# Kernel tuning notes

Measured on AMD Instinct MI355X. Metric: run time of the kernel, lower is better.

Reference implementation:

```python
import jax, jax.numpy as jnp
import numpy as np

HEADS1, HID1 = 4, 64   # layer 1: concat -> 256
HEADS2, HID2 = 1, 64   # layer 2: out_channels
NEG_SLOPE = 0.2


def gat_layer(x_src, x_dst, W_src, W_dst, att_src, att_dst, bias, src, dst, n_tgt, heads, hid):
    # bipartite GATConv (PyG math), concat heads
    xs = (x_src @ W_src).reshape(-1, heads, hid)          # [Ns,H,C]
    xd = (x_dst @ W_dst).reshape(-1, heads, hid)          # [Nt,H,C]
    a_s = jnp.sum(xs * att_src, axis=-1)                  # [Ns,H]
    a_d = jnp.sum(xd * att_dst, axis=-1)                  # [Nt,H]
    e = jax.nn.leaky_relu(a_s[src] + a_d[dst], NEG_SLOPE) # [E,H]
    m = jax.ops.segment_max(e, dst, num_segments=n_tgt)
    m = jnp.where(jnp.isfinite(m), m, 0.0)
    ex = jnp.exp(e - m[dst])
    denom = jax.ops.segment_sum(ex, dst, num_segments=n_tgt)
    alpha = ex / (denom[dst] + 1e-16)                     # edge softmax per target
    msg = xs[src] * alpha[:, :, None]                     # [E,H,C]
    out = jax.ops.segment_sum(msg, dst, num_segments=n_tgt)
    return out.reshape(n_tgt, heads * hid) + bias


def setup_inputs() -> dict:
    key = jax.random.key(0)
    ks = jax.random.split(key, 20)
    N0, NT1, NT2 = 100000, 25000, 5000
    E1, E2 = 400000, 100000
    IN, H1 = 256, HEADS1 * HID1  # 256
    OUT = HEADS2 * HID2          # 64
    g = lambda k, sh, fan: jax.random.normal(k, sh, jnp.float32) * (1.0 / np.sqrt(fan))
    return {
        'x': jax.random.normal(ks[0], (N0, IN), jnp.float32),
        'src1': jax.random.randint(ks[1], (E1,), 0, N0),
        'dst1': jax.random.randint(ks[2], (E1,), 0, NT1),
        'src2': jax.random.randint(ks[3], (E2,), 0, NT1),
        'dst2': jax.random.randint(ks[4], (E2,), 0, NT2),
        'n_tgt1': NT1, 'n_tgt2': NT2,
        'W1_src': g(ks[5], (IN, H1), IN), 'W1_dst': g(ks[6], (IN, H1), IN),
        'att1_src': g(ks[7], (HEADS1, HID1), HID1), 'att1_dst': g(ks[8], (HEADS1, HID1), HID1),
        'bias1': jnp.zeros((H1,), jnp.float32),
        'skip1_W': g(ks[9], (IN, H1), IN), 'skip1_b': jnp.zeros((H1,), jnp.float32),
        'W2_src': g(ks[10], (H1, OUT), H1), 'W2_dst': g(ks[11], (H1, OUT), H1),
        'att2_src': g(ks[12], (HEADS2, HID2), HID2), 'att2_dst': g(ks[13], (HEADS2, HID2), HID2),
        'bias2': jnp.zeros((OUT,), jnp.float32),
        'skip2_W': g(ks[14], (H1, OUT), H1), 'skip2_b': jnp.zeros((OUT,), jnp.float32),
    }


def reference(x, src1, dst1, src2, dst2, n_tgt1, n_tgt2,
              W1_src, W1_dst, att1_src, att1_dst, bias1, skip1_W, skip1_b,
              W2_src, W2_dst, att2_src, att2_dst, bias2, skip2_W, skip2_b):
    # layer 1: conv + skip + elu (dropout inactive in eval)
    x_t1 = x[:n_tgt1]
    h = gat_layer(x, x_t1, W1_src, W1_dst, att1_src, att1_dst, bias1,
                  src1, dst1, n_tgt1, HEADS1, HID1)
    h = h + (x_t1 @ skip1_W + skip1_b)
    h = jax.nn.elu(h)
    # layer 2 (final): conv + skip, then log_softmax
    x_t2 = h[:n_tgt2]
    o = gat_layer(h, x_t2, W2_src, W2_dst, att2_src, att2_dst, bias2,
                  src2, dst2, n_tgt2, HEADS2, HID2)
    o = o + (x_t2 @ skip2_W + skip2_b)
    return jax.nn.log_softmax(o, axis=-1)
```

## Files before the change

### kernel.cpp

```cpp
#include <hip/hip_runtime.h>
#include <hip/hip_bf16.h>

using bf16 = __hip_bfloat16;
typedef __attribute__((ext_vector_type(8))) short short8;
typedef __attribute__((ext_vector_type(4))) short short4v;
typedef __attribute__((ext_vector_type(4))) float float4v;

__device__ __forceinline__ short f2bs(float x) {
    bf16 b = __float2bfloat16(x);
    return __builtin_bit_cast(short, b);
}
__device__ __forceinline__ float bs2f(short s) {
    return __uint_as_float(((unsigned)(unsigned short)s) << 16);
}
__device__ __forceinline__ void glds16(const void* g, void* l) {
    __builtin_amdgcn_global_load_lds(
        (const __attribute__((address_space(1))) unsigned int*)g,
        (__attribute__((address_space(3))) unsigned int*)l, 16, 0, 0);
}

__global__ __launch_bounds__(256) void gemm_l1(
        const float* __restrict__ A, const bf16* __restrict__ Bt,
        bf16* __restrict__ xs1, bf16* __restrict__ sk1,
        float* __restrict__ as1, float* __restrict__ ad1,
        const float* __restrict__ att_s, const float* __restrict__ att_d,
        int M, int NT) {
    __shared__ short lds[16 * 512];
    __shared__ float red[128][2];
    const int y = blockIdx.y;
    const int row0 = blockIdx.x * 128;
    if (y >= 2 && row0 >= NT) return;
    const int col0 = y * 128;
    const int tid = threadIdx.x;
    const int wave = tid >> 6, lane = tid & 63;
    const int quad = lane >> 4, l16 = lane & 15;
    const int wr = wave >> 1, wc = wave & 1;

    const float4v fz = {0.f, 0.f, 0.f, 0.f};
    float4v acc[4][4];
#pragma unroll
    for (int i = 0; i < 4; i++)
#pragma unroll
        for (int j = 0; j < 4; j++) acc[i][j] = fz;

    for (int kit = 0; kit < 8; kit++) {
        const int k0 = kit * 32;
        float4v f0[2], f1[2];
#pragma unroll
        for (int i = 0; i < 2; i++) {
            int ar = row0 + (wave * 2 + i) * 16 + l16;
            ar = ar < M ? ar : M - 1;
            const float4v* p = (const float4v*)&A[(size_t)ar * 256 + k0 + quad * 8];
            f0[i] = p[0];
            f1[i] = p[1];
        }
#pragma unroll
        for (int i = 0; i < 2; i++) {
            int bb = wave * 2 + i;
            int brow = col0 + bb * 16 + l16;
            glds16(&Bt[(size_t)brow * 256 + k0 + quad * 8], &lds[(8 + bb) * 512]);
        }
#pragma unroll
        for (int i = 0; i < 2; i++) {
            short8 v;
#pragma unroll
            for (int j = 0; j < 4; j++) { v[j] = f2bs(f0[i][j]); v[4 + j] = f2bs(f1[i][j]); }
            *(short8*)&lds[(wave * 2 + i) * 512 + lane * 8] = v;
        }
        __syncthreads();
        short8 afr[4], bfr[4];
#pragma unroll
        for (int mi = 0; mi < 4; mi++)
            afr[mi] = *(short8*)&lds[(wr * 4 + mi) * 512 + lane * 8];
#pragma unroll
        for (int ni = 0; ni < 4; ni++)
            bfr[ni] = *(short8*)&lds[(8 + wc * 4 + ni) * 512 + lane * 8];
#pragma unroll
        for (int mi = 0; mi < 4; mi++)
#pragma unroll
            for (int ni = 0; ni < 4; ni++)
                acc[mi][ni] = __builtin_amdgcn_mfma_f32_16x16x32_bf16(
                    afr[mi], bfr[ni], acc[mi][ni], 0, 0, 0);
        __syncthreads();
    }

    if (y < 4) {
        const float* attc = y < 2 ? att_s : att_d;
        const int hb = (y < 2 ? y * 2 : (y - 2) * 2) + wc;
        float av[4];
#pragma unroll
        for (int ni = 0; ni < 4; ni++) av[ni] = attc[hb * 64 + ni * 16 + l16];
#pragma unroll
        for (int mi = 0; mi < 4; mi++) {
#pragma unroll
            for (int r = 0; r < 4; r++) {
                float t = acc[mi][0][r] * av[0] + acc[mi][1][r] * av[1] +
                          acc[mi][2][r] * av[2] + acc[mi][3][r] * av[3];
                t += __shfl_xor(t, 1, 64);
                t += __shfl_xor(t, 2, 64);
                t += __shfl_xor(t, 4, 64);
                t += __shfl_xor(t, 8, 64);
                if (l16 == 0) red[wr * 64 + mi * 16 + quad * 4 + r][wc] = t;
            }
        }
        __syncthreads();
        const int aM = y < 2 ? M : NT;
        float* aout = y < 2 ? as1 : ad1;
        const int hbase = y < 2 ? y * 2 : (y - 2) * 2;
        int rl = tid >> 1, gl = tid & 1;
        int grow = row0 + rl;
        if (grow < aM) aout[(size_t)grow * 4 + hbase + gl] = red[rl][gl];
    }

    if (y < 2) {
#pragma unroll
        for (int mi = 0; mi < 4; mi++)
#pragma unroll
            for (int ni = 0; ni < 4; ni++) {
                int col = col0 + wc * 64 + ni * 16 + l16;
#pragma unroll
                for (int r = 0; r < 4; r++) {
                    int row = row0 + wr * 64 + mi * 16 + quad * 4 + r;
                    if (row < M)
                        xs1[(size_t)row * 256 + col] = __float2bfloat16(acc[mi][ni][r]);
                }
            }
    } else if (y >= 4) {
#pragma unroll
        for (int mi = 0; mi < 4; mi++)
#pragma unroll
            for (int ni = 0; ni < 4; ni++) {
                int scol = col0 - 512 + wc * 64 + ni * 16 + l16;
#pragma unroll
                for (int r = 0; r < 4; r++) {
                    int row = row0 + wr * 64 + mi * 16 + quad * 4 + r;
                    if (row < NT)
                        sk1[(size_t)row * 256 + scol] = __float2bfloat16(acc[mi][ni][r]);
                }
            }
    }
}

__global__ __launch_bounds__(256) void gemm_l2(
        const bf16* __restrict__ Ah, const bf16* __restrict__ Bt,
        float* __restrict__ x2, float* __restrict__ a2,
        const float* __restrict__ attc, int NT) {
    __shared__ short lds[12 * 512];
    __shared__ float red[128];
    const int y = blockIdx.y;
    const int row0 = blockIdx.x * 128;
    const int col0 = y * 64;
    const int tid = threadIdx.x;
    const int wave = tid >> 6, lane = tid & 63;
    const int quad = lane >> 4, l16 = lane & 15;

    const float4v fz = {0.f, 0.f, 0.f, 0.f};
    float4v acc[2][4];
#pragma unroll
    for (int i = 0; i < 2; i++)
#pragma unroll
        for (int j = 0; j < 4; j++) acc[i][j] = fz;

    for (int kit = 0; kit < 8; kit++) {
        const int k0 = kit * 32;
#pragma unroll
        for (int i = 0; i < 3; i++) {
            int b = wave * 3 + i;
            if (b < 8) {
                glds16(&Ah[(size_t)(row0 + b * 16 + l16) * 256 + k0 + quad * 8],
                       &lds[b * 512]);
            } else {
                int bb = b - 8;
                glds16(&Bt[(size_t)(col0 + bb * 16 + l16) * 256 + k0 + quad * 8],
                       &lds[b * 512]);
            }
        }
        __syncthreads();
        short8 afr[2], bfr[4];
#pragma unroll
        for (int mi = 0; mi < 2; mi++)
            afr[mi] = *(short8*)&lds[(wave * 2 + mi) * 512 + lane * 8];
#pragma unroll
        for (int ni = 0; ni < 4; ni++)
            bfr[ni] = *(short8*)&lds[(8 + ni) * 512 + lane * 8];
#pragma unroll
        for (int mi = 0; mi < 2; mi++)
#pragma unroll
            for (int ni = 0; ni < 4; ni++)
                acc[mi][ni] = __builtin_amdgcn_mfma_f32_16x16x32_bf16(
                    afr[mi], bfr[ni], acc[mi][ni], 0, 0, 0);
        __syncthreads();
    }

    if (y < 2) {
        float av[4];
#pragma unroll
        for (int ni = 0; ni < 4; ni++) av[ni] = attc[y * 64 + ni * 16 + l16];
#pragma unroll
        for (int mi = 0; mi < 2; mi++) {
#pragma unroll
            for (int r = 0; r < 4; r++) {
                float t = acc[mi][0][r] * av[0] + acc[mi][1][r] * av[1] +
                          acc[mi][2][r] * av[2] + acc[mi][3][r] * av[3];
                t += __shfl_xor(t, 1, 64);
                t += __shfl_xor(t, 2, 64);
                t += __shfl_xor(t, 4, 64);
                t += __shfl_xor(t, 8, 64);
                if (l16 == 0) red[wave * 32 + mi * 16 + quad * 4 + r] = t;
            }
        }
        __syncthreads();
        if (tid < 128) {
            int grow = row0 + tid;
            if (grow < NT) a2[(size_t)grow * 2 + y] = red[tid];
        }
    }
#pragma unroll
    for (int mi = 0; mi < 2; mi++)
#pragma unroll
        for (int ni = 0; ni < 4; ni++) {
            int col = col0 + ni * 16 + l16;
#pragma unroll
            for (int r = 0; r < 4; r++) {
                int row = row0 + wave * 32 + mi * 16 + quad * 4 + r;
                if (row < NT) x2[(size_t)row * 192 + col] = acc[mi][ni][r];
            }
        }
}

__global__ void prep_all(const float* __restrict__ W1s, const float* __restrict__ W1d,
                         const float* __restrict__ W1sk, const float* __restrict__ W2s,
                         const float* __restrict__ W2d, const float* __restrict__ W2sk,
                         const float* __restrict__ a2s, const float* __restrict__ a2d,
                         bf16* __restrict__ Wt1, bf16* __restrict__ Wt2,
                         float* __restrict__ at2c, int* __restrict__ fills, int nfill) {
    int t = blockIdx.x * blockDim.x + threadIdx.x;
    if (t < 196608) {
        int n = t >> 8, k = t & 255;
        const float* W = n < 256 ? W1s : (n < 512 ? W1d : W1sk);
        Wt1[t] = __float2bfloat16(W[k * 256 + (n & 255)]);
    } else if (t < 245760) {
        int i = t - 196608;
        int n = i >> 8, k = i & 255;
        const float* W = n < 64 ? W2s : (n < 128 ? W2d : W2sk);
        Wt2[i] = __float2bfloat16(W[k * 64 + (n & 63)]);
    } else if (t < 245888) {
        int i = t - 245760;
        at2c[i] = i < 64 ? a2s[i] : a2d[i - 64];
    } else if (t < 245888 + nfill) {
        fills[t - 245888] = 0;
    }
}

__global__ void bucket_scatter(const int* __restrict__ s1, const int* __restrict__ d1, int E1,
                               const int* __restrict__ s2, const int* __restrict__ d2, int E2,
                               int* __restrict__ fill1, int* __restrict__ fill2,
                               int* __restrict__ psrc1, int* __restrict__ psrc2) {
    int t = blockIdx.x * blockDim.x + threadIdx.x;
    if (t < E1) {
        int d = d1[t];
        int pos = atomicAdd(&fill1[d], 1);
        if (pos < 64) psrc1[(d << 6) + pos] = s1[t];
    } else if (t < E1 + E2) {
        int tt = t - E1;
        int d = d2[tt];
        int pos = atomicAdd(&fill2[d], 1);
        if (pos < 64) psrc2[(d << 6) + pos] = s2[tt];
    }
}

__global__ __launch_bounds__(256) void agg_h4(
        const int* __restrict__ fill, const int* __restrict__ psrc,
        const bf16* __restrict__ X, const float* __restrict__ as1,
        const float* __restrict__ ad1, const float* __restrict__ bias,
        const bf16* __restrict__ skip, const float* __restrict__ skipb,
        bf16* __restrict__ h) {
    __shared__ float exl[4][64][4];
    __shared__ float red[4][256];
    const int d = blockIdx.x;
    const int tid = threadIdx.x;
    const int wv = tid >> 6, lane = tid & 63;
    const int head = lane >> 4;
    int deg = fill[d];
    deg = deg < 64 ? deg : 64;
    int se = 0;
    float4v ex4 = {0.f, 0.f, 0.f, 0.f};
    const float4v ad4 = *(const float4v*)&ad1[(size_t)d * 4];
    if (lane < deg) {
        se = psrc[((size_t)d << 6) + lane];
        float4v as4 = *(const float4v*)&as1[(size_t)se * 4];
#pragma unroll
        for (int c = 0; c < 4; c++) {
            float v = as4[c] + ad4[c];
            v = v > 0.f ? v : 0.2f * v;
            ex4[c] = expf(v);
        }
    }
    *(float4v*)&exl[wv][lane][0] = ex4;
    float4v dn = ex4;
#pragma unroll
    for (int o = 32; o; o >>= 1) {
        dn.x += __shfl_xor(dn.x, o, 64);
        dn.y += __shfl_xor(dn.y, o, 64);
        dn.z += __shfl_xor(dn.z, o, 64);
        dn.w += __shfl_xor(dn.w, o, 64);
    }
    float4v acc = {0.f, 0.f, 0.f, 0.f}, acc2 = {0.f, 0.f, 0.f, 0.f};
    int p = wv;
    for (; p + 4 < deg; p += 8) {
        int sA = __shfl(se, p, 64), sB = __shfl(se, p + 4, 64);
        float aA = exl[wv][p][head], aB = exl[wv][p + 4][head];
        short4v xa = *(const short4v*)&X[(size_t)sA * 256 + lane * 4];
        short4v xb = *(const short4v*)&X[(size_t)sB * 256 + lane * 4];
        acc.x += bs2f(xa.x) * aA; acc2.x += bs2f(xb.x) * aB;
        acc.y += bs2f(xa.y) * aA; acc2.y += bs2f(xb.y) * aB;
        acc.z += bs2f(xa.z) * aA; acc2.z += bs2f(xb.z) * aB;
        acc.w += bs2f(xa.w) * aA; acc2.w += bs2f(xb.w) * aB;
    }
    for (; p < deg; p += 4) {
        int sA = __shfl(se, p, 64);
        float aA = exl[wv][p][head];
        short4v xa = *(const short4v*)&X[(size_t)sA * 256 + lane * 4];
        acc.x += bs2f(xa.x) * aA;
        acc.y += bs2f(xa.y) * aA;
        acc.z += bs2f(xa.z) * aA;
        acc.w += bs2f(xa.w) * aA;
    }
    acc.x += acc2.x; acc.y += acc2.y; acc.z += acc2.z; acc.w += acc2.w;
    *(float4v*)&red[wv][lane * 4] = acc;
    __syncthreads();
    const int f = tid;
    float sum = red[0][f] + red[1][f] + red[2][f] + red[3][f];
    int hf = f >> 6;
    float den = hf == 0 ? dn.x : hf == 1 ? dn.y : hf == 2 ? dn.z : dn.w;
    float v = sum / (den + 1e-16f) + bias[f] + __bfloat162float(skip[(size_t)d * 256 + f]) +
              skipb[f];
    h[(size_t)d * 256 + f] = __float2bfloat16(v > 0.f ? v : expm1f(v));
}

__global__ __launch_bounds__(256) void agg_h1(
        const int* __restrict__ fill2, const int* __restrict__ psrc2,
        const float* __restrict__ x2, const float* __restrict__ a2,
        const float* __restrict__ bias, const float* __restrict__ skipb,
        float* __restrict__ out, int M) {
    const int d = blockIdx.x * 4 + (threadIdx.x >> 6);
    const int lane = threadIdx.x & 63;
    if (d >= M) return;
    int deg = fill2[d];
    deg = deg < 64 ? deg : 64;
    int se = 0;
    float exv = 0.f;
    const float adv = a2[(size_t)d * 2 + 1];
    if (lane < deg) {
        se = psrc2[((size_t)d << 6) + lane];
        float v = a2[(size_t)se * 2] + adv;
        v = v > 0.f ? v : 0.2f * v;
        exv = expf(v);
    }
    float den = exv;
#pragma unroll
    for (int o = 32; o; o >>= 1) den += __shfl_xor(den, o, 64);
    float acc = 0.f, acc2 = 0.f;
    int p = 0;
    for (; p + 1 < deg; p += 2) {
        int sA = __shfl(se, p, 64), sB = __shfl(se, p + 1, 64);
        float aA = __shfl(exv, p, 64), aB = __shfl(exv, p + 1, 64);
        acc += x2[(size_t)sA * 192 + lane] * aA;
        acc2 += x2[(size_t)sB * 192 + lane] * aB;
    }
    if (p < deg) {
        int sA = __shfl(se, p, 64);
        acc += x2[(size_t)sA * 192 + lane] * __shfl(exv, p, 64);
    }
    float v = (acc + acc2) / (den + 1e-16f) + bias[lane] +
              x2[(size_t)d * 192 + 128 + lane] + skipb[lane];
    float m = v;
#pragma unroll
    for (int o = 32; o; o >>= 1) m = fmaxf(m, __shfl_xor(m, o, 64));
    float e = expf(v - m);
#pragma unroll
    for (int o = 32; o; o >>= 1) e += __shfl_xor(e, o, 64);
    out[(size_t)d * 64 + lane] = v - m - logf(e);
}

extern "C" void kernel_launch(void* const* d_in, const int* in_sizes, int n_in,
                              void* d_out, int out_size, void* d_ws, size_t ws_size,
                              hipStream_t stream) {
    const float* x        = (const float*)d_in[0];
    const int*   src1     = (const int*)d_in[1];
    const int*   dst1     = (const int*)d_in[2];
    const int*   src2     = (const int*)d_in[3];
    const int*   dst2     = (const int*)d_in[4];
    const float* W1_src   = (const float*)d_in[7];
    const float* W1_dst   = (const float*)d_in[8];
    const float* att1_src = (const float*)d_in[9];
    const float* att1_dst = (const float*)d_in[10];
    const float* bias1    = (const float*)d_in[11];
    const float* skip1_W  = (const float*)d_in[12];
    const float* skip1_b  = (const float*)d_in[13];
    const float* W2_src   = (const float*)d_in[14];
    const float* W2_dst   = (const float*)d_in[15];
    const float* att2_src = (const float*)d_in[16];
    const float* att2_dst = (const float*)d_in[17];
    const float* bias2    = (const float*)d_in[18];
    const float* skip2_W  = (const float*)d_in[19];
    const float* skip2_b  = (const float*)d_in[20];

    const int N0  = in_sizes[0] / 256;
    const int E1  = in_sizes[1];
    const int E2  = in_sizes[3];
    const int NT1 = 25000, NT2 = 5000;
    const int NT1p = 25088;

    char* ws = (char*)d_ws;
    size_t off = 0;
    auto alloc = [&](size_t b) { size_t o = off; off += (b + 255) & ~(size_t)255; return o; };
    size_t o_xs1   = alloc((size_t)N0 * 256 * 2);
    size_t o_sk1   = alloc((size_t)NT1 * 256 * 2);
    size_t o_h     = alloc((size_t)NT1p * 256 * 2);
    size_t o_as1   = alloc((size_t)N0 * 4 * 4);
    size_t o_ad1   = alloc((size_t)NT1 * 4 * 4);
    size_t o_fill  = alloc((size_t)(NT1 + NT2) * 4);
    size_t o_psrc1 = alloc((size_t)NT1 * 64 * 4);
    size_t o_psrc2 = alloc((size_t)NT2 * 64 * 4);
    size_t o_wt1   = alloc((size_t)768 * 256 * 2);
    size_t o_wt2   = alloc((size_t)192 * 256 * 2);
    size_t o_at2c  = alloc((size_t)128 * 4);
    size_t off2a = o_xs1;
    auto alloc2 = [&](size_t b) { size_t o = off2a; off2a += (b + 255) & ~(size_t)255; return o; };
    size_t o_x2 = alloc2((size_t)NT1 * 192 * 4);
    size_t o_a2 = alloc2((size_t)NT1 * 2 * 4);

    bf16*  xs1   = (bf16*)(ws + o_xs1);
    bf16*  sk1   = (bf16*)(ws + o_sk1);
    bf16*  h     = (bf16*)(ws + o_h);
    float* as1   = (float*)(ws + o_as1);
    float* ad1   = (float*)(ws + o_ad1);
    int*   fill1 = (int*)(ws + o_fill);
    int*   fill2 = fill1 + NT1;
    int*   psrc1 = (int*)(ws + o_psrc1);
    int*   psrc2 = (int*)(ws + o_psrc2);
    bf16*  Wt1   = (bf16*)(ws + o_wt1);
    bf16*  Wt2   = (bf16*)(ws + o_wt2);
    float* at2c  = (float*)(ws + o_at2c);
    float* x2    = (float*)(ws + o_x2);
    float* a2    = (float*)(ws + o_a2);

    prep_all<<<(245888 + NT1 + NT2 + 255) / 256, 256, 0, stream>>>(
        W1_src, W1_dst, skip1_W, W2_src, W2_dst, skip2_W, att2_src, att2_dst,
        Wt1, Wt2, at2c, fill1, NT1 + NT2);
    bucket_scatter<<<(E1 + E2 + 255) / 256, 256, 0, stream>>>(
        src1, dst1, E1, src2, dst2, E2, fill1, fill2, psrc1, psrc2);
    gemm_l1<<<dim3((N0 + 127) / 128, 6), 256, 0, stream>>>(
        x, Wt1, xs1, sk1, as1, ad1, att1_src, att1_dst, N0, NT1);
    agg_h4<<<NT1, 256, 0, stream>>>(fill1, psrc1, xs1, as1, ad1, bias1, sk1, skip1_b, h);
    gemm_l2<<<dim3((NT1 + 127) / 128, 3), 256, 0, stream>>>(h, Wt2, x2, a2, at2c, NT1);
    agg_h1<<<(NT2 + 3) / 4, 256, 0, stream>>>(fill2, psrc2, x2, a2, bias2, skip2_b,
                                              (float*)d_out, NT2);
}
```

Measured before the change: 350.3 us.

## Double-buffer LDS tiles in both GEMM kernels to overlap loads with MFMA

```diff
diff --git a/kernel.cpp b/kernel.cpp
--- a/kernel.cpp
+++ b/kernel.cpp
@@ -25,7 +25,7 @@
         float* __restrict__ as1, float* __restrict__ ad1,
         const float* __restrict__ att_s, const float* __restrict__ att_d,
         int M, int NT) {
-    __shared__ short lds[16 * 512];
+    __shared__ short lds[2][16 * 512];
     __shared__ float red[128][2];
     const int y = blockIdx.y;
     const int row0 = blockIdx.x * 128;
@@ -43,44 +43,72 @@
 #pragma unroll
         for (int j = 0; j < 4; j++) acc[i][j] = fz;
 
+    float4v f0[2], f1[2];
+#pragma unroll
+    for (int i = 0; i < 2; i++) {
+        int ar = row0 + (wave * 2 + i) * 16 + l16;
+        ar = ar < M ? ar : M - 1;
+        const float4v* p = (const float4v*)&A[(size_t)ar * 256 + quad * 8];
+        f0[i] = p[0];
+        f1[i] = p[1];
+    }
+#pragma unroll
+    for (int i = 0; i < 2; i++) {
+        int bb = wave * 2 + i;
+        glds16(&Bt[(size_t)(col0 + bb * 16 + l16) * 256 + quad * 8],
+               &lds[0][(8 + bb) * 512]);
+    }
+#pragma unroll
+    for (int i = 0; i < 2; i++) {
+        short8 v;
+#pragma unroll
+        for (int j = 0; j < 4; j++) { v[j] = f2bs(f0[i][j]); v[4 + j] = f2bs(f1[i][j]); }
+        *(short8*)&lds[0][(wave * 2 + i) * 512 + lane * 8] = v;
+    }
+    __syncthreads();
+
+#pragma unroll
     for (int kit = 0; kit < 8; kit++) {
-        const int k0 = kit * 32;
-        float4v f0[2], f1[2];
-#pragma unroll
-        for (int i = 0; i < 2; i++) {
-            int ar = row0 + (wave * 2 + i) * 16 + l16;
-            ar = ar < M ? ar : M - 1;
-            const float4v* p = (const float4v*)&A[(size_t)ar * 256 + k0 + quad * 8];
-            f0[i] = p[0];
-            f1[i] = p[1];
-        }
-#pragma unroll
-        for (int i = 0; i < 2; i++) {
-            int bb = wave * 2 + i;
-            int brow = col0 + bb * 16 + l16;
-            glds16(&Bt[(size_t)brow * 256 + k0 + quad * 8], &lds[(8 + bb) * 512]);
-        }
-#pragma unroll
-        for (int i = 0; i < 2; i++) {
-            short8 v;
-#pragma unroll
-            for (int j = 0; j < 4; j++) { v[j] = f2bs(f0[i][j]); v[4 + j] = f2bs(f1[i][j]); }
-            *(short8*)&lds[(wave * 2 + i) * 512 + lane * 8] = v;
-        }
-        __syncthreads();
+        const int cur = kit & 1, nxt = cur ^ 1;
+        if (kit < 7) {
+            const int k0 = (kit + 1) * 32;
+#pragma unroll
+            for (int i = 0; i < 2; i++) {
+                int ar = row0 + (wave * 2 + i) * 16 + l16;
+                ar = ar < M ? ar : M - 1;
+                const float4v* p = (const float4v*)&A[(size_t)ar * 256 + k0 + quad * 8];
+                f0[i] = p[0];
+                f1[i] = p[1];
+            }
+#pragma unroll
+            for (int i = 0; i < 2; i++) {
+                int bb = wave * 2 + i;
+                glds16(&Bt[(size_t)(col0 + bb * 16 + l16) * 256 + k0 + quad * 8],
+                       &lds[nxt][(8 + bb) * 512]);
+            }
+        }
         short8 afr[4], bfr[4];
 #pragma unroll
         for (int mi = 0; mi < 4; mi++)
-            afr[mi] = *(short8*)&lds[(wr * 4 + mi) * 512 + lane * 8];
+            afr[mi] = *(short8*)&lds[cur][(wr * 4 + mi) * 512 + lane * 8];
 #pragma unroll
         for (int ni = 0; ni < 4; ni++)
-            bfr[ni] = *(short8*)&lds[(8 + wc * 4 + ni) * 512 + lane * 8];
+            bfr[ni] = *(short8*)&lds[cur][(8 + wc * 4 + ni) * 512 + lane * 8];
 #pragma unroll
         for (int mi = 0; mi < 4; mi++)
 #pragma unroll
             for (int ni = 0; ni < 4; ni++)
                 acc[mi][ni] = __builtin_amdgcn_mfma_f32_16x16x32_bf16(
                     afr[mi], bfr[ni], acc[mi][ni], 0, 0, 0);
+        if (kit < 7) {
+#pragma unroll
+            for (int i = 0; i < 2; i++) {
+                short8 v;
+#pragma unroll
+                for (int j = 0; j < 4; j++) { v[j] = f2bs(f0[i][j]); v[4 + j] = f2bs(f1[i][j]); }
+                *(short8*)&lds[nxt][(wave * 2 + i) * 512 + lane * 8] = v;
+            }
+        }
         __syncthreads();
     }
 
@@ -145,7 +173,7 @@
         const bf16* __restrict__ Ah, const bf16* __restrict__ Bt,
         float* __restrict__ x2, float* __restrict__ a2,
         const float* __restrict__ attc, int NT) {
-    __shared__ short lds[12 * 512];
+    __shared__ short lds[2][12 * 512];
     __shared__ float red[128];
     const int y = blockIdx.y;
     const int row0 = blockIdx.x * 128;
@@ -161,28 +189,43 @@
 #pragma unroll
         for (int j = 0; j < 4; j++) acc[i][j] = fz;
 
+#pragma unroll
+    for (int i = 0; i < 3; i++) {
+        int b = wave * 3 + i;
+        if (b < 8) {
+            glds16(&Ah[(size_t)(row0 + b * 16 + l16) * 256 + quad * 8], &lds[0][b * 512]);
+        } else {
+            int bb = b - 8;
+            glds16(&Bt[(size_t)(col0 + bb * 16 + l16) * 256 + quad * 8], &lds[0][b * 512]);
+        }
+    }
+    __syncthreads();
+
+#pragma unroll
     for (int kit = 0; kit < 8; kit++) {
-        const int k0 = kit * 32;
-#pragma unroll
-        for (int i = 0; i < 3; i++) {
-            int b = wave * 3 + i;
-            if (b < 8) {
-                glds16(&Ah[(size_t)(row0 + b * 16 + l16) * 256 + k0 + quad * 8],
-                       &lds[b * 512]);
-            } else {
-                int bb = b - 8;
-                glds16(&Bt[(size_t)(col0 + bb * 16 + l16) * 256 + k0 + quad * 8],
-                       &lds[b * 512]);
-            }
-        }
-        __syncthreads();
+        const int cur = kit & 1, nxt = cur ^ 1;
+        if (kit < 7) {
+            const int k0 = (kit + 1) * 32;
+#pragma unroll
+            for (int i = 0; i < 3; i++) {
+                int b = wave * 3 + i;
+                if (b < 8) {
+                    glds16(&Ah[(size_t)(row0 + b * 16 + l16) * 256 + k0 + quad * 8],
+                           &lds[nxt][b * 512]);
+                } else {
+                    int bb = b - 8;
+                    glds16(&Bt[(size_t)(col0 + bb * 16 + l16) * 256 + k0 + quad * 8],
+                           &lds[nxt][b * 512]);
+                }
+            }
+        }
         short8 afr[2], bfr[4];
 #pragma unroll
         for (int mi = 0; mi < 2; mi++)
-            afr[mi] = *(short8*)&lds[(wave * 2 + mi) * 512 + lane * 8];
+            afr[mi] = *(short8*)&lds[cur][(wave * 2 + mi) * 512 + lane * 8];
 #pragma unroll
         for (int ni = 0; ni < 4; ni++)
-            bfr[ni] = *(short8*)&lds[(8 + ni) * 512 + lane * 8];
+            bfr[ni] = *(short8*)&lds[cur][(8 + ni) * 512 + lane * 8];
 #pragma unroll
         for (int mi = 0; mi < 2; mi++)
 #pragma unroll
```

Result: no change. 355.8 us (+1.6%).

## Preload full B tile into LDS and stream A via registers in GEMMs

Applied to the files above, without the earlier changes.

```diff
diff --git a/kernel.cpp b/kernel.cpp
--- a/kernel.cpp
+++ b/kernel.cpp
@@ -19,14 +19,13 @@
         (__attribute__((address_space(3))) unsigned int*)l, 16, 0, 0);
 }
 
-__global__ __launch_bounds__(256) void gemm_l1(
+__global__ __launch_bounds__(512, 4) void gemm_l1(
         const float* __restrict__ A, const bf16* __restrict__ Bt,
         bf16* __restrict__ xs1, bf16* __restrict__ sk1,
         float* __restrict__ as1, float* __restrict__ ad1,
         const float* __restrict__ att_s, const float* __restrict__ att_d,
         int M, int NT) {
-    __shared__ short lds[16 * 512];
-    __shared__ float red[128][2];
+    __shared__ short ldsB[64 * 512];
     const int y = blockIdx.y;
     const int row0 = blockIdx.x * 128;
     if (y >= 2 && row0 >= NT) return;
@@ -34,119 +33,101 @@
     const int tid = threadIdx.x;
     const int wave = tid >> 6, lane = tid & 63;
     const int quad = lane >> 4, l16 = lane & 15;
-    const int wr = wave >> 1, wc = wave & 1;
+
+#pragma unroll
+    for (int kit = 0; kit < 8; kit++)
+        glds16(&Bt[(size_t)(col0 + wave * 16 + l16) * 256 + kit * 32 + quad * 8],
+               &ldsB[(wave * 8 + kit) * 512]);
+
+    const int arow_ = row0 + wave * 16 + l16;
+    const int arow = arow_ < M ? arow_ : M - 1;
+    const float* Ap = &A[(size_t)arow * 256 + quad * 8];
 
     const float4v fz = {0.f, 0.f, 0.f, 0.f};
-    float4v acc[4][4];
-#pragma unroll
-    for (int i = 0; i < 4; i++)
-#pragma unroll
-        for (int j = 0; j < 4; j++) acc[i][j] = fz;
-
+    float4v acc[8];
+#pragma unroll
+    for (int n = 0; n < 8; n++) acc[n] = fz;
+
+    __syncthreads();
+
+    float4v pf0[4], pf1[4];
+#pragma unroll
+    for (int i = 0; i < 4; i++) {
+        pf0[i] = *(const float4v*)(Ap + i * 32);
+        pf1[i] = *(const float4v*)(Ap + i * 32 + 4);
+    }
+
+#pragma unroll
     for (int kit = 0; kit < 8; kit++) {
-        const int k0 = kit * 32;
-        float4v f0[2], f1[2];
-#pragma unroll
-        for (int i = 0; i < 2; i++) {
-            int ar = row0 + (wave * 2 + i) * 16 + l16;
-            ar = ar < M ? ar : M - 1;
-            const float4v* p = (const float4v*)&A[(size_t)ar * 256 + k0 + quad * 8];
-            f0[i] = p[0];
-            f1[i] = p[1];
-        }
-#pragma unroll
-        for (int i = 0; i < 2; i++) {
-            int bb = wave * 2 + i;
-            int brow = col0 + bb * 16 + l16;
-            glds16(&Bt[(size_t)brow * 256 + k0 + quad * 8], &lds[(8 + bb) * 512]);
-        }
-#pragma unroll
-        for (int i = 0; i < 2; i++) {
-            short8 v;
-#pragma unroll
-            for (int j = 0; j < 4; j++) { v[j] = f2bs(f0[i][j]); v[4 + j] = f2bs(f1[i][j]); }
-            *(short8*)&lds[(wave * 2 + i) * 512 + lane * 8] = v;
-        }
-        __syncthreads();
-        short8 afr[4], bfr[4];
-#pragma unroll
-        for (int mi = 0; mi < 4; mi++)
-            afr[mi] = *(short8*)&lds[(wr * 4 + mi) * 512 + lane * 8];
-#pragma unroll
-        for (int ni = 0; ni < 4; ni++)
-            bfr[ni] = *(short8*)&lds[(8 + wc * 4 + ni) * 512 + lane * 8];
-#pragma unroll
-        for (int mi = 0; mi < 4; mi++)
-#pragma unroll
-            for (int ni = 0; ni < 4; ni++)
-                acc[mi][ni] = __builtin_amdgcn_mfma_f32_16x16x32_bf16(
-                    afr[mi], bfr[ni], acc[mi][ni], 0, 0, 0);
-        __syncthreads();
-    }
+        const int s = kit & 3;
+        short8 af;
+#pragma unroll
+        for (int j = 0; j < 4; j++) { af[j] = f2bs(pf0[s][j]); af[4 + j] = f2bs(pf1[s][j]); }
+        if (kit < 4) {
+            pf0[s] = *(const float4v*)(Ap + (kit + 4) * 32);
+            pf1[s] = *(const float4v*)(Ap + (kit + 4) * 32 + 4);
+        }
+#pragma unroll
+        for (int n = 0; n < 8; n++) {
+            short8 bf = *(short8*)&ldsB[(n * 8 + kit) * 512 + lane * 8];
+            acc[n] = __builtin_amdgcn_mfma_f32_16x16x32_bf16(af, bf, acc[n], 0, 0, 0);
+        }
+    }
+
+    const int rbase = row0 + wave * 16 + quad * 4;
 
     if (y < 4) {
         const float* attc = y < 2 ? att_s : att_d;
-        const int hb = (y < 2 ? y * 2 : (y - 2) * 2) + wc;
-        float av[4];
-#pragma unroll
-        for (int ni = 0; ni < 4; ni++) av[ni] = attc[hb * 64 + ni * 16 + l16];
-#pragma unroll
-        for (int mi = 0; mi < 4; mi++) {
+        const int hbase = y < 2 ? y * 2 : (y - 2) * 2;
+        const int aM = y < 2 ? M : NT;
+        float* aout = y < 2 ? as1 : ad1;
+#pragma unroll
+        for (int h = 0; h < 2; h++) {
+            float av[4];
+#pragma unroll
+            for (int n = 0; n < 4; n++) av[n] = attc[(hbase + h) * 64 + n * 16 + l16];
 #pragma unroll
             for (int r = 0; r < 4; r++) {
-                float t = acc[mi][0][r] * av[0] + acc[mi][1][r] * av[1] +
-                          acc[mi][2][r] * av[2] + acc[mi][3][r] * av[3];
+                float t = acc[h * 4 + 0][r] * av[0] + acc[h * 4 + 1][r] * av[1] +
+                          acc[h * 4 + 2][r] * av[2] + acc[h * 4 + 3][r] * av[3];
                 t += __shfl_xor(t, 1, 64);
                 t += __shfl_xor(t, 2, 64);
                 t += __shfl_xor(t, 4, 64);
                 t += __shfl_xor(t, 8, 64);
-                if (l16 == 0) red[wr * 64 + mi * 16 + quad * 4 + r][wc] = t;
+                int grow = rbase + r;
+                if (l16 == 0 && grow < aM) aout[(size_t)grow * 4 + hbase + h] = t;
             }
         }
-        __syncthreads();
-        const int aM = y < 2 ? M : NT;
-        float* aout = y < 2 ? as1 : ad1;
-        const int hbase = y < 2 ? y * 2 : (y - 2) * 2;
-        int rl = tid >> 1, gl = tid & 1;
-        int grow = row0 + rl;
-        if (grow < aM) aout[(size_t)grow * 4 + hbase + gl] = red[rl][gl];
     }
 
     if (y < 2) {
 #pragma unroll
-        for (int mi = 0; mi < 4; mi++)
-#pragma unroll
-            for (int ni = 0; ni < 4; ni++) {
-                int col = col0 + wc * 64 + ni * 16 + l16;
-#pragma unroll
-                for (int r = 0; r < 4; r++) {
-                    int row = row0 + wr * 64 + mi * 16 + quad * 4 + r;
-                    if (row < M)
-                        xs1[(size_t)row * 256 + col] = __float2bfloat16(acc[mi][ni][r]);
-                }
+        for (int n = 0; n < 8; n++) {
+            int col = col0 + n * 16 + l16;
+#pragma unroll
+            for (int r = 0; r < 4; r++) {
+                int row = rbase + r;
+                if (row < M) xs1[(size_t)row * 256 + col] = __float2bfloat16(acc[n][r]);
             }
+        }
     } else if (y >= 4) {
 #pragma unroll
-        for (int mi = 0; mi < 4; mi++)
-#pragma unroll
-            for (int ni = 0; ni < 4; ni++) {
-                int scol = col0 - 512 + wc * 64 + ni * 16 + l16;
-#pragma unroll
-                for (int r = 0; r < 4; r++) {
-                    int row = row0 + wr * 64 + mi * 16 + quad * 4 + r;
-                    if (row < NT)
-                        sk1[(size_t)row * 256 + scol] = __float2bfloat16(acc[mi][ni][r]);
-                }
+        for (int n = 0; n < 8; n++) {
+            int scol = col0 - 512 + n * 16 + l16;
+#pragma unroll
+            for (int r = 0; r < 4; r++) {
+                int row = rbase + r;
+                if (row < NT) sk1[(size_t)row * 256 + scol] = __float2bfloat16(acc[n][r]);
             }
-    }
-}
-
-__global__ __launch_bounds__(256) void gemm_l2(
+        }
+    }
+}
+
+__global__ __launch_bounds__(512, 4) void gemm_l2(
         const bf16* __restrict__ Ah, const bf16* __restrict__ Bt,
         float* __restrict__ x2, float* __restrict__ a2,
         const float* __restrict__ attc, int NT) {
-    __shared__ short lds[12 * 512];
-    __shared__ float red[128];
+    __shared__ short ldsB[32 * 512];
     const int y = blockIdx.y;
     const int row0 = blockIdx.x * 128;
     const int col0 = y * 64;
@@ -154,78 +135,64 @@
     const int wave = tid >> 6, lane = tid & 63;
     const int quad = lane >> 4, l16 = lane & 15;
 
+#pragma unroll
+    for (int i = 0; i < 4; i++) {
+        int blk = wave * 4 + i;
+        int cb = blk >> 3, kit = blk & 7;
+        glds16(&Bt[(size_t)(col0 + cb * 16 + l16) * 256 + kit * 32 + quad * 8],
+               &ldsB[blk * 512]);
+    }
+
+    const int arow = row0 + wave * 16 + l16;
+    const bf16* Ap = &Ah[(size_t)arow * 256 + quad * 8];
+
     const float4v fz = {0.f, 0.f, 0.f, 0.f};
-    float4v acc[2][4];
-#pragma unroll
-    for (int i = 0; i < 2; i++)
-#pragma unroll
-        for (int j = 0; j < 4; j++) acc[i][j] = fz;
-
+    float4v acc[4];
+#pragma unroll
+    for (int n = 0; n < 4; n++) acc[n] = fz;
+
+    __syncthreads();
+
+    short8 s[8];
+#pragma unroll
+    for (int kit = 0; kit < 8; kit++) s[kit] = *(const short8*)(Ap + kit * 32);
+
+#pragma unroll
     for (int kit = 0; kit < 8; kit++) {
-        const int k0 = kit * 32;
-#pragma unroll
-        for (int i = 0; i < 3; i++) {
-            int b = wave * 3 + i;
-            if (b < 8) {
-                glds16(&Ah[(size_t)(row0 + b * 16 + l16) * 256 + k0 + quad * 8],
-                       &lds[b * 512]);
-            } else {
-                int bb = b - 8;
-                glds16(&Bt[(size_t)(col0 + bb * 16 + l16) * 256 + k0 + quad * 8],
-                       &lds[b * 512]);
-            }
-        }
-        __syncthreads();
-        short8 afr[2], bfr[4];
-#pragma unroll
-        for (int mi = 0; mi < 2; mi++)
-            afr[mi] = *(short8*)&lds[(wave * 2 + mi) * 512 + lane * 8];
-#pragma unroll
-        for (int ni = 0; ni < 4; ni++)
-            bfr[ni] = *(short8*)&lds[(8 + ni) * 512 + lane * 8];
-#pragma unroll
-        for (int mi = 0; mi < 2; mi++)
-#pragma unroll
-            for (int ni = 0; ni < 4; ni++)
-                acc[mi][ni] = __builtin_amdgcn_mfma_f32_16x16x32_bf16(
-                    afr[mi], bfr[ni], acc[mi][ni], 0, 0, 0);
-        __syncthreads();
-    }
+#pragma unroll
+        for (int n = 0; n < 4; n++) {
+            short8 bf = *(short8*)&ldsB[(n * 8 + kit) * 512 + lane * 8];
+            acc[n] = __builtin_amdgcn_mfma_f32_16x16x32_bf16(s[kit], bf, acc[n], 0, 0, 0);
+        }
+    }
+
+    const int rbase = row0 + wave * 16 + quad * 4;
 
     if (y < 2) {
         float av[4];
 #pragma unroll
-        for (int ni = 0; ni < 4; ni++) av[ni] = attc[y * 64 + ni * 16 + l16];
-#pragma unroll
-        for (int mi = 0; mi < 2; mi++) {
-#pragma unroll
-            for (int r = 0; r < 4; r++) {
-                float t = acc[mi][0][r] * av[0] + acc[mi][1][r] * av[1] +
-                          acc[mi][2][r] * av[2] + acc[mi][3][r] * av[3];
-                t += __shfl_xor(t, 1, 64);
-                t += __shfl_xor(t, 2, 64);
-                t += __shfl_xor(t, 4, 64);
-                t += __shfl_xor(t, 8, 64);
-                if (l16 == 0) red[wave * 32 + mi * 16 + quad * 4 + r] = t;
-            }
-        }
-        __syncthreads();
-        if (tid < 128) {
-            int grow = row0 + tid;
-            if (grow < NT) a2[(size_t)grow * 2 + y] = red[tid];
-        }
-    }
-#pragma unroll
-    for (int mi = 0; mi < 2; mi++)
-#pragma unroll
-        for (int ni = 0; ni < 4; ni++) {
-            int col = col0 + ni * 16 + l16;
-#pragma unroll
-            for (int r = 0; r < 4; r++) {
-                int row = row0 + wave * 32 + mi * 16 + quad * 4 + r;
-                if (row < NT) x2[(size_t)row * 192 + col] = acc[mi][ni][r];
-            }
-        }
+        for (int n = 0; n < 4; n++) av[n] = attc[y * 64 + n * 16 + l16];
+#pragma unroll
+        for (int r = 0; r < 4; r++) {
+            float t = acc[0][r] * av[0] + acc[1][r] * av[1] +
+                      acc[2][r] * av[2] + acc[3][r] * av[3];
+            t += __shfl_xor(t, 1, 64);
+            t += __shfl_xor(t, 2, 64);
+            t += __shfl_xor(t, 4, 64);
+            t += __shfl_xor(t, 8, 64);
+            int grow = rbase + r;
+            if (l16 == 0 && grow < NT) a2[(size_t)grow * 2 + y] = t;
+        }
+    }
+#pragma unroll
+    for (int n = 0; n < 4; n++) {
+        int col = col0 + n * 16 + l16;
+#pragma unroll
+        for (int r = 0; r < 4; r++) {
+            int row = rbase + r;
+            if (row < NT) x2[(size_t)row * 192 + col] = acc[n][r];
+        }
+    }
 }
 
 __global__ void prep_all(const float* __restrict__ W1s, const float* __restrict__ W1d,
@@ -451,10 +418,10 @@
         Wt1, Wt2, at2c, fill1, NT1 + NT2);
     bucket_scatter<<<(E1 + E2 + 255) / 256, 256, 0, stream>>>(
         src1, dst1, E1, src2, dst2, E2, fill1, fill2, psrc1, psrc2);
-    gemm_l1<<<dim3((N0 + 127) / 128, 6), 256, 0, stream>>>(
+    gemm_l1<<<dim3((N0 + 127) / 128, 6), 512, 0, stream>>>(
         x, Wt1, xs1, sk1, as1, ad1, att1_src, att1_dst, N0, NT1);
     agg_h4<<<NT1, 256, 0, stream>>>(fill1, psrc1, xs1, as1, ad1, bias1, sk1, skip1_b, h);
-    gemm_l2<<<dim3((NT1 + 127) / 128, 3), 256, 0, stream>>>(h, Wt2, x2, a2, at2c, NT1);
+    gemm_l2<<<dim3((NT1 + 127) / 128, 3), 512, 0, stream>>>(h, Wt2, x2, a2, at2c, NT1);
     agg_h1<<<(NT2 + 3) / 4, 256, 0, stream>>>(fill2, psrc2, x2, a2, bias2, skip2_b,
                                               (float*)d_out, NT2);
 }
```

After: 351.1 us. No clear change (+0.2%).
